# Optimization experiments

Hardware: AMD Instinct MI355X
Metric: run time of the kernel (lower is better)

The kernel has to match this reference:

```python
import jax, jax.numpy as jnp
import numpy as np

NUM_SAMPLES = 1024


def _cdist(a, b):
    # a, b: (n, 3) -> (n, n) pairwise euclidean distances (torch.cdist p=2)
    d2 = jnp.sum((a[:, None, :] - b[None, :, :]) ** 2, axis=-1)
    return jnp.sqrt(jnp.maximum(d2, 0.0))


def _greedy_match_cost(cost):
    # Greedy sequential matching: repeatedly take the global argmin over
    # still-unmatched rows/cols, accumulate its cost, eliminate row+col.
    n = cost.shape[0]

    def step(carry, _):
        row_mask, col_mask, loss = carry
        valid = row_mask[:, None] & col_mask[None, :]
        masked = jnp.where(valid, cost, jnp.inf)
        idx = jnp.argmin(masked)  # row-major first-min == torch's min(dim=1)+argmin tiebreak
        r = idx // n
        c = idx % n
        loss = loss + cost[r, c]
        return (row_mask.at[r].set(False), col_mask.at[c].set(False), loss), None

    init = (jnp.ones((n,), dtype=bool), jnp.ones((n,), dtype=bool), jnp.float32(0.0))
    (_, _, loss), _ = jax.lax.scan(step, init, None, length=n)
    return loss / n


def setup_inputs() -> dict:
    key = jax.random.key(0)
    k1, k2, k3 = jax.random.split(key, 3)
    B, N, n = 8, 4096, NUM_SAMPLES
    S1 = jax.random.normal(k1, (B, N, 3), dtype=jnp.float32)
    S2 = jax.random.normal(k2, (B, N, 3), dtype=jnp.float32)
    # torch.randperm(N)[:n] per batch element: without-replacement sampling
    perm_keys = jax.random.split(k3, B)
    indices = jax.vmap(lambda k: jax.random.permutation(k, N)[:n])(perm_keys).astype(jnp.int32)
    return {"S1": S1, "S2": S2, "indices": indices}


def reference(S1, S2, indices):
    # sample the same indices from both sets, per batch (matches original loop)
    s1 = jnp.take_along_axis(S1, indices[:, :, None], axis=1)  # (B, n, 3)
    s2 = jnp.take_along_axis(S2, indices[:, :, None], axis=1)  # (B, n, 3)
    cost = jax.vmap(_cdist)(s1, s2)  # (B, n, n)
    losses = jax.vmap(_greedy_match_cost)(cost)  # (B,)
    return jnp.mean(losses)
```

## Files before the change

kernel.cpp:

```cpp
#include <hip/hip_runtime.h>
#include <stdint.h>

#define BATCH 8
#define NPTS 4096
#define NS 1024
#define KD 6

typedef unsigned long long u64;
typedef unsigned int u32;
typedef unsigned short u16;
typedef unsigned char u8;

#define DEADV (~0ull)
#define QNANB 0x7FC00000u

__device__ __forceinline__ float pdist3(float ax, float ay, float az,
                                        float bx, float by, float bz) {
    float dx = ax - bx, dy = ay - by, dz = az - bz;
    float d2 = __fmaf_rn(dz, dz, __fmaf_rn(dy, dy, dx * dx));
    return __fsqrt_rn(d2);
}

__device__ __forceinline__ u64 packv(float d, u32 row, u32 col) {
    return ((u64)__float_as_uint(d) << 20) | ((u64)row << 10) | (u64)col;
}

__device__ __forceinline__ u64 u64min2(u64 a, u64 b) { return a < b ? a : b; }
__device__ __forceinline__ u64 u64max2(u64 a, u64 b) { return a > b ? a : b; }

__device__ __forceinline__ u64 tree16(const u64* p) {
    u64 a0 = u64min2(p[0], p[1]),   a1 = u64min2(p[2], p[3]);
    u64 a2 = u64min2(p[4], p[5]),   a3 = u64min2(p[6], p[7]);
    u64 a4 = u64min2(p[8], p[9]),   a5 = u64min2(p[10], p[11]);
    u64 a6 = u64min2(p[12], p[13]), a7 = u64min2(p[14], p[15]);
    u64 b0 = u64min2(a0, a1), b1 = u64min2(a2, a3);
    u64 b2 = u64min2(a4, a5), b3 = u64min2(a6, a7);
    return u64min2(u64min2(b0, b1), u64min2(b2, b3));
}

template<int CTRL>
__device__ __forceinline__ u64 dpp_min_step(u64 m) {
    u32 lo = (u32)m, hi = (u32)(m >> 32);
    u32 olo = (u32)__builtin_amdgcn_update_dpp(-1, (int)lo, CTRL, 0xF, 0xF, false);
    u32 ohi = (u32)__builtin_amdgcn_update_dpp(-1, (int)hi, CTRL, 0xF, 0xF, false);
    u64 o = ((u64)ohi << 32) | olo;
    return o < m ? o : m;
}

__device__ __forceinline__ u64 wave_min_u64(u64 m) {
    m = dpp_min_step<0x111>(m);
    m = dpp_min_step<0x112>(m);
    m = dpp_min_step<0x114>(m);
    m = dpp_min_step<0x118>(m);
    m = dpp_min_step<0x142>(m);
    m = dpp_min_step<0x143>(m);
    u32 lo = (u32)__builtin_amdgcn_readlane((int)(u32)m, 63);
    u32 hi = (u32)__builtin_amdgcn_readlane((int)(u32)(m >> 32), 63);
    return ((u64)hi << 32) | lo;
}

__global__ void gather_k(const float* __restrict__ S1, const float* __restrict__ S2,
                         const int* __restrict__ idx,
                         float4* __restrict__ s1g, float4* __restrict__ s2g) {
    int t = blockIdx.x * blockDim.x + threadIdx.x;
    if (t >= BATCH * NS) return;
    int b = t >> 10;
    int j = idx[t];
    const float* p1 = S1 + ((size_t)b * NPTS + j) * 3;
    const float* p2 = S2 + ((size_t)b * NPTS + j) * 3;
    s1g[t] = make_float4(p1[0], p1[1], p1[2], 0.f);
    s2g[t] = make_float4(p2[0], p2[1], p2[2], 0.f);
}

__global__ void lists_k(const float4* __restrict__ s1g, const float4* __restrict__ s2g,
                        u64* __restrict__ rlist_g, u64* __restrict__ clist_g) {
    int gg = blockIdx.x * 4 + (threadIdx.x >> 6);
    int lane = threadIdx.x & 63;
    int side = (gg >= BATCH * NS) ? 1 : 0;
    int g = gg - side * (BATCH * NS);
    int b = g >> 10;
    u32 rc = (u32)(g & 1023);
    float4 a = side ? s2g[g] : s1g[g];
    const float4* other = (side ? s1g : s2g) + (size_t)b * NS;
    u64 cand[16];
    #pragma unroll
    for (int k = 0; k < 16; ++k) {
        int o = lane + (k << 6);
        float4 q = other[o];
        float d = pdist3(a.x, a.y, a.z, q.x, q.y, q.z);
        cand[k] = side ? packv(d, (u32)o, rc) : packv(d, rc, (u32)o);
    }
    u64* out = (side ? clist_g : rlist_g) + (size_t)g * KD;
    for (int i = 0; i < KD; ++i) {
        u64 m1 = wave_min_u64(tree16(cand));
        if (lane == 0) out[i] = m1;
        #pragma unroll
        for (int k = 0; k < 16; ++k) cand[k] = (cand[k] == m1) ? DEADV : cand[k];
    }
}

__global__ void __launch_bounds__(1024, 1)
resolve_k(const float4* __restrict__ s1g, const float4* __restrict__ s2g,
          const u64* __restrict__ rlist_gl, const u64* __restrict__ clist_gl,
          float* __restrict__ loss_ws) {
    __shared__ u64 rlist[NS * KD];
    __shared__ u64 clist[NS * KD];
    __shared__ u64 rmin[NS];
    __shared__ u64 cmin[NS];
    __shared__ float s1xs[NS], s1ys[NS], s1zs[NS];
    __shared__ float s2xs[NS], s2ys[NS], s2zs[NS];
    __shared__ u8 rptrs[NS], cptrs[NS];
    __shared__ u16 qrow[NS], qcol[NS];
    __shared__ u16 lrows[NS], lcols[NS];
    __shared__ float lred[1024];
    __shared__ int qrn, qcn, matched, nlr, nlc;
    int b = blockIdx.x;
    int tid = threadIdx.x;
    int lane = tid & 63, wv = tid >> 6;

    {
        const float4* rs = (const float4*)(rlist_gl + (size_t)b * NS * KD);
        const float4* cs = (const float4*)(clist_gl + (size_t)b * NS * KD);
        float4* rd = (float4*)rlist;
        float4* cd = (float4*)clist;
        for (int i = tid; i < NS * KD / 2; i += 1024) { rd[i] = rs[i]; cd[i] = cs[i]; }
    }
    {
        float4 v1 = s1g[(size_t)b * NS + tid];
        s1xs[tid] = v1.x; s1ys[tid] = v1.y; s1zs[tid] = v1.z;
        float4 v2 = s2g[(size_t)b * NS + tid];
        s2xs[tid] = v2.x; s2ys[tid] = v2.y; s2zs[tid] = v2.z;
    }
    rptrs[tid] = 1; cptrs[tid] = 1;
    if (tid == 0) matched = 0;
    __syncthreads();
    rmin[tid] = rlist[tid * KD];
    cmin[tid] = clist[tid * KD];
    float loss = 0.f;
    __syncthreads();

    for (int round = 0; round < NS; ++round) {
        u64 myk = rmin[tid];
        u32 c = (u32)myk & 1023u;
        bool mut = (myk != DEADV) && (cmin[c] == myk);
        __syncthreads();
        if (mut) {
            loss += __uint_as_float((u32)(myk >> 20));
            rmin[tid] = DEADV;
            cmin[c] = DEADV;
            s1xs[tid] = __uint_as_float(QNANB);
            s2xs[c]   = __uint_as_float(QNANB);
        }
        u64 bal = __ballot((int)mut);
        if (lane == 0 && bal) atomicAdd(&matched, (int)__popcll(bal));
        if (tid == 0) { qrn = 0; qcn = 0; nlr = 0; nlc = 0; }
        __syncthreads();
        if (matched >= NS) break;
        u64 rk = rmin[tid];
        if (rk != DEADV) {
            float pr = s2xs[(u32)rk & 1023u];
            if (pr != pr) {
                u32 p = rptrs[tid];
                bool found = false;
                while (p < KD) {
                    u64 e = rlist[tid * KD + p];
                    ++p;
                    if (e != DEADV) {
                        float q = s2xs[(u32)e & 1023u];
                        if (q == q) { rmin[tid] = e; found = true; break; }
                    }
                }
                rptrs[tid] = (u8)p;
                if (!found) { int s = atomicAdd(&qrn, 1); qrow[s] = (u16)tid; }
            }
        }
        u64 ck = cmin[tid];
        if (ck != DEADV) {
            float pr = s1xs[((u32)ck >> 10) & 1023u];
            if (pr != pr) {
                u32 p = cptrs[tid];
                bool found = false;
                while (p < KD) {
                    u64 e = clist[tid * KD + p];
                    ++p;
                    if (e != DEADV) {
                        float q = s1xs[((u32)e >> 10) & 1023u];
                        if (q == q) { cmin[tid] = e; found = true; break; }
                    }
                }
                cptrs[tid] = (u8)p;
                if (!found) { int s = atomicAdd(&qcn, 1); qcol[s] = (u16)tid; }
            }
        }
        {
            bool calive = (s2xs[tid] == s2xs[tid]);
            u64 cb = __ballot((int)calive);
            int crank = (int)__popcll(cb & ((1ull << lane) - 1ull));
            int cbase = 0;
            if (lane == 0) cbase = atomicAdd(&nlc, (int)__popcll(cb));
            cbase = __shfl(cbase, 0, 64);
            if (calive) lcols[cbase + crank] = (u16)tid;

            bool ralive = (s1xs[tid] == s1xs[tid]);
            u64 rb = __ballot((int)ralive);
            int rrank = (int)__popcll(rb & ((1ull << lane) - 1ull));
            int rbase = 0;
            if (lane == 0) rbase = atomicAdd(&nlr, (int)__popcll(rb));
            rbase = __shfl(rbase, 0, 64);
            if (ralive) lrows[rbase + rrank] = (u16)tid;
        }
        __syncthreads();
        int nr = qrn, nc = qcn;
        int nlcv = nlc, nlrv = nlr;
        for (int qi = wv; qi < nr; qi += 16) {
            u32 r = qrow[qi];
            float ax = s1xs[r], ay = s1ys[r], az = s1zs[r];
            u64 m1 = DEADV, m2 = DEADV;
            for (int i = lane; i < nlcv; i += 64) {
                int cc = lcols[i];
                float d = pdist3(ax, ay, az, s2xs[cc], s2ys[cc], s2zs[cc]);
                u64 p = packv(d, r, (u32)cc);
                u64 mx = u64max2(p, m1);
                m1 = u64min2(m1, p);
                m2 = u64min2(m2, mx);
            }
            u64 M1 = wave_min_u64(m1);
            u64 c2 = (m1 == M1) ? m2 : m1;
            u64 M2 = wave_min_u64(c2);
            if (lane == 0) {
                rmin[r] = M1;
                rlist[r * KD + KD - 1] = M2;
                rptrs[r] = KD - 1;
            }
        }
        for (int qi = wv; qi < nc; qi += 16) {
            u32 cc = qcol[qi];
            float ax = s2xs[cc], ay = s2ys[cc], az = s2zs[cc];
            u64 m1 = DEADV, m2 = DEADV;
            for (int i = lane; i < nlrv; i += 64) {
                int r = lrows[i];
                float d = pdist3(s1xs[r], s1ys[r], s1zs[r], ax, ay, az);
                u64 p = packv(d, (u32)r, cc);
                u64 mx = u64max2(p, m1);
                m1 = u64min2(m1, p);
                m2 = u64min2(m2, mx);
            }
            u64 M1 = wave_min_u64(m1);
            u64 c2 = (m1 == M1) ? m2 : m1;
            u64 M2 = wave_min_u64(c2);
            if (lane == 0) {
                cmin[cc] = M1;
                clist[cc * KD + KD - 1] = M2;
                cptrs[cc] = KD - 1;
            }
        }
        __syncthreads();
    }

    lred[tid] = loss;
    __syncthreads();
    #pragma unroll
    for (int s = 512; s > 0; s >>= 1) {
        if (tid < s) lred[tid] += lred[tid + s];
        __syncthreads();
    }
    if (tid == 0) loss_ws[b] = lred[0] * (1.0f / NS);
}

__global__ void finish_k(const float* __restrict__ loss_ws, float* __restrict__ out) {
    if (threadIdx.x == 0) {
        float s = 0.f;
        for (int i = 0; i < BATCH; ++i) s += loss_ws[i];
        out[0] = s * (1.0f / BATCH);
    }
}

extern "C" void kernel_launch(void* const* d_in, const int* in_sizes, int n_in,
                              void* d_out, int out_size, void* d_ws, size_t ws_size,
                              hipStream_t stream) {
    const float* S1 = (const float*)d_in[0];
    const float* S2 = (const float*)d_in[1];
    const int* idx  = (const int*)d_in[2];
    char* ws = (char*)d_ws;
    size_t o = 0;
    float4* s1g    = (float4*)(ws + o); o += (size_t)BATCH * NS * 16;
    float4* s2g    = (float4*)(ws + o); o += (size_t)BATCH * NS * 16;
    u64* rlist_g   = (u64*)(ws + o);    o += (size_t)BATCH * NS * KD * 8;
    u64* clist_g   = (u64*)(ws + o);    o += (size_t)BATCH * NS * KD * 8;
    float* loss_ws = (float*)(ws + o);

    gather_k<<<(BATCH * NS + 255) / 256, 256, 0, stream>>>(S1, S2, idx, s1g, s2g);
    lists_k<<<2 * BATCH * NS / 4, 256, 0, stream>>>(s1g, s2g, rlist_g, clist_g);
    resolve_k<<<BATCH, 1024, 0, stream>>>(s1g, s2g, rlist_g, clist_g, loss_ws);
    finish_k<<<1, 64, 0, stream>>>(loss_ws, (float*)d_out);
}
```

Before: 204.6 us.

## Lazily rebuild alive lists, pack coords as float4, fuse final reduction

```diff
diff --git a/kernel.cpp b/kernel.cpp
--- a/kernel.cpp
+++ b/kernel.cpp
@@ -61,8 +61,10 @@
 
 __global__ void gather_k(const float* __restrict__ S1, const float* __restrict__ S2,
                          const int* __restrict__ idx,
-                         float4* __restrict__ s1g, float4* __restrict__ s2g) {
+                         float4* __restrict__ s1g, float4* __restrict__ s2g,
+                         int* __restrict__ cnt) {
     int t = blockIdx.x * blockDim.x + threadIdx.x;
+    if (t == 0) *cnt = 0;
     if (t >= BATCH * NS) return;
     int b = t >> 10;
     int j = idx[t];
@@ -102,18 +104,19 @@
 __global__ void __launch_bounds__(1024, 1)
 resolve_k(const float4* __restrict__ s1g, const float4* __restrict__ s2g,
           const u64* __restrict__ rlist_gl, const u64* __restrict__ clist_gl,
-          float* __restrict__ loss_ws) {
+          float* __restrict__ loss_ws, int* __restrict__ cnt,
+          float* __restrict__ out) {
     __shared__ u64 rlist[NS * KD];
     __shared__ u64 clist[NS * KD];
     __shared__ u64 rmin[NS];
     __shared__ u64 cmin[NS];
-    __shared__ float s1xs[NS], s1ys[NS], s1zs[NS];
-    __shared__ float s2xs[NS], s2ys[NS], s2zs[NS];
+    __shared__ float4 s1p[NS];
+    __shared__ float4 s2p[NS];
     __shared__ u8 rptrs[NS], cptrs[NS];
     __shared__ u16 qrow[NS], qcol[NS];
     __shared__ u16 lrows[NS], lcols[NS];
     __shared__ float lred[1024];
-    __shared__ int qrn, qcn, matched, nlr, nlc;
+    __shared__ int qrn, qcn, matched, nlr, nlc, stale_n;
     int b = blockIdx.x;
     int tid = threadIdx.x;
     int lane = tid & 63, wv = tid >> 6;
@@ -125,14 +128,11 @@
         float4* cd = (float4*)clist;
         for (int i = tid; i < NS * KD / 2; i += 1024) { rd[i] = rs[i]; cd[i] = cs[i]; }
     }
-    {
-        float4 v1 = s1g[(size_t)b * NS + tid];
-        s1xs[tid] = v1.x; s1ys[tid] = v1.y; s1zs[tid] = v1.z;
-        float4 v2 = s2g[(size_t)b * NS + tid];
-        s2xs[tid] = v2.x; s2ys[tid] = v2.y; s2zs[tid] = v2.z;
-    }
+    s1p[tid] = s1g[(size_t)b * NS + tid];
+    s2p[tid] = s2g[(size_t)b * NS + tid];
     rptrs[tid] = 1; cptrs[tid] = 1;
-    if (tid == 0) matched = 0;
+    lrows[tid] = (u16)tid; lcols[tid] = (u16)tid;
+    if (tid == 0) { matched = 0; stale_n = NS; }
     __syncthreads();
     rmin[tid] = rlist[tid * KD];
     cmin[tid] = clist[tid * KD];
@@ -148,17 +148,21 @@
             loss += __uint_as_float((u32)(myk >> 20));
             rmin[tid] = DEADV;
             cmin[c] = DEADV;
-            s1xs[tid] = __uint_as_float(QNANB);
-            s2xs[c]   = __uint_as_float(QNANB);
+            s1p[tid].x = __uint_as_float(QNANB);
+            s2p[c].x   = __uint_as_float(QNANB);
         }
         u64 bal = __ballot((int)mut);
         if (lane == 0 && bal) atomicAdd(&matched, (int)__popcll(bal));
         if (tid == 0) { qrn = 0; qcn = 0; nlr = 0; nlc = 0; }
         __syncthreads();
-        if (matched >= NS) break;
+        int m = matched;
+        if (m >= NS) break;
+        int live = NS - m;
+        int stale = stale_n;
+        bool rebuild = (stale * 4 > live * 5 + 64);
         u64 rk = rmin[tid];
         if (rk != DEADV) {
-            float pr = s2xs[(u32)rk & 1023u];
+            float pr = s2p[(u32)rk & 1023u].x;
             if (pr != pr) {
                 u32 p = rptrs[tid];
                 bool found = false;
@@ -166,7 +170,7 @@
                     u64 e = rlist[tid * KD + p];
                     ++p;
                     if (e != DEADV) {
-                        float q = s2xs[(u32)e & 1023u];
+                        float q = s2p[(u32)e & 1023u].x;
                         if (q == q) { rmin[tid] = e; found = true; break; }
                     }
                 }
@@ -176,7 +180,7 @@
         }
         u64 ck = cmin[tid];
         if (ck != DEADV) {
-            float pr = s1xs[((u32)ck >> 10) & 1023u];
+            float pr = s1p[((u32)ck >> 10) & 1023u].x;
             if (pr != pr) {
                 u32 p = cptrs[tid];
                 bool found = false;
@@ -184,7 +188,7 @@
                     u64 e = clist[tid * KD + p];
                     ++p;
                     if (e != DEADV) {
-                        float q = s1xs[((u32)e >> 10) & 1023u];
+                        float q = s1p[((u32)e >> 10) & 1023u].x;
                         if (q == q) { cmin[tid] = e; found = true; break; }
                     }
                 }
@@ -192,8 +196,9 @@
                 if (!found) { int s = atomicAdd(&qcn, 1); qcol[s] = (u16)tid; }
             }
         }
-        {
-            bool calive = (s2xs[tid] == s2xs[tid]);
+        if (rebuild) {
+            float cx = s2p[tid].x;
+            bool calive = (cx == cx);
             u64 cb = __ballot((int)calive);
             int crank = (int)__popcll(cb & ((1ull << lane) - 1ull));
             int cbase = 0;
@@ -201,7 +206,8 @@
             cbase = __shfl(cbase, 0, 64);
             if (calive) lcols[cbase + crank] = (u16)tid;
 
-            bool ralive = (s1xs[tid] == s1xs[tid]);
+            float rx = s1p[tid].x;
+            bool ralive = (rx == rx);
             u64 rb = __ballot((int)ralive);
             int rrank = (int)__popcll(rb & ((1ull << lane) - 1ull));
             int rbase = 0;
@@ -211,14 +217,16 @@
         }
         __syncthreads();
         int nr = qrn, nc = qcn;
-        int nlcv = nlc, nlrv = nlr;
+        int scan_n = rebuild ? live : stale;
+        if (rebuild && tid == 0) stale_n = live;
         for (int qi = wv; qi < nr; qi += 16) {
             u32 r = qrow[qi];
-            float ax = s1xs[r], ay = s1ys[r], az = s1zs[r];
+            float4 a = s1p[r];
             u64 m1 = DEADV, m2 = DEADV;
-            for (int i = lane; i < nlcv; i += 64) {
+            for (int i = lane; i < scan_n; i += 64) {
                 int cc = lcols[i];
-                float d = pdist3(ax, ay, az, s2xs[cc], s2ys[cc], s2zs[cc]);
+                float4 q = s2p[cc];
+                float d = pdist3(a.x, a.y, a.z, q.x, q.y, q.z);
                 u64 p = packv(d, r, (u32)cc);
                 u64 mx = u64max2(p, m1);
                 m1 = u64min2(m1, p);
@@ -235,11 +243,12 @@
         }
         for (int qi = wv; qi < nc; qi += 16) {
             u32 cc = qcol[qi];
-            float ax = s2xs[cc], ay = s2ys[cc], az = s2zs[cc];
+            float4 a = s2p[cc];
             u64 m1 = DEADV, m2 = DEADV;
-            for (int i = lane; i < nlrv; i += 64) {
+            for (int i = lane; i < scan_n; i += 64) {
                 int r = lrows[i];
-                float d = pdist3(s1xs[r], s1ys[r], s1zs[r], ax, ay, az);
+                float4 q = s1p[r];
+                float d = pdist3(q.x, q.y, q.z, a.x, a.y, a.z);
                 u64 p = packv(d, (u32)r, cc);
                 u64 mx = u64max2(p, m1);
                 m1 = u64min2(m1, p);
@@ -264,14 +273,16 @@
         if (tid < s) lred[tid] += lred[tid + s];
         __syncthreads();
     }
-    if (tid == 0) loss_ws[b] = lred[0] * (1.0f / NS);
-}
-
-__global__ void finish_k(const float* __restrict__ loss_ws, float* __restrict__ out) {
-    if (threadIdx.x == 0) {
-        float s = 0.f;
-        for (int i = 0; i < BATCH; ++i) s += loss_ws[i];
-        out[0] = s * (1.0f / BATCH);
+    if (tid == 0) {
+        atomicExch(&loss_ws[b], lred[0] * (1.0f / NS));
+        __threadfence();
+        int old = atomicAdd(cnt, 1);
+        if (old == BATCH - 1) {
+            __threadfence();
+            float s = 0.f;
+            for (int i = 0; i < BATCH; ++i) s += atomicAdd(&loss_ws[i], 0.0f);
+            out[0] = s * (1.0f / BATCH);
+        }
     }
 }
 
@@ -287,10 +298,11 @@
     float4* s2g    = (float4*)(ws + o); o += (size_t)BATCH * NS * 16;
     u64* rlist_g   = (u64*)(ws + o);    o += (size_t)BATCH * NS * KD * 8;
     u64* clist_g   = (u64*)(ws + o);    o += (size_t)BATCH * NS * KD * 8;
-    float* loss_ws = (float*)(ws + o);
-
-    gather_k<<<(BATCH * NS + 255) / 256, 256, 0, stream>>>(S1, S2, idx, s1g, s2g);
+    float* loss_ws = (float*)(ws + o);  o += (size_t)BATCH * 4;
+    int* cnt       = (int*)(ws + o);
+
+    gather_k<<<(BATCH * NS + 255) / 256, 256, 0, stream>>>(S1, S2, idx, s1g, s2g, cnt);
     lists_k<<<2 * BATCH * NS / 4, 256, 0, stream>>>(s1g, s2g, rlist_g, clist_g);
-    resolve_k<<<BATCH, 1024, 0, stream>>>(s1g, s2g, rlist_g, clist_g, loss_ws);
-    finish_k<<<1, 64, 0, stream>>>(loss_ws, (float*)d_out);
-}
+    resolve_k<<<BATCH, 1024, 0, stream>>>(s1g, s2g, rlist_g, clist_g, loss_ws, cnt,
+                                          (float*)d_out);
+}
```

After: 198.8 us. -2.8%, faster.
